# Performance work log

Hardware: AMD Instinct MI355X
Metric: run time of the kernel (lower is better)

Reference implementation:

```python
import jax, jax.numpy as jnp
import numpy as np

B, T, D, N, H = 2, 2048, 2048, 16, 128
WINDOW = 1024
SOFT_CAP = 50.0
K_MASK = -2.3819763e+38
MAX_WAVELENGTH = 10000


def apply_rope(x, positions, head_dim):
    # x: [B, T, N, H], positions: [B, T]
    fraction = 2.0 * jnp.arange(head_dim // 2, dtype=jnp.float32) / head_dim
    timescale = MAX_WAVELENGTH ** fraction                      # [H/2]
    sinusoid = positions[..., None].astype(jnp.float32) / timescale  # [B, T, H/2]
    sinusoid = sinusoid[..., None, :]                           # [B, T, 1, H/2]
    sin, cos = jnp.sin(sinusoid), jnp.cos(sinusoid)
    first, second = jnp.split(x, 2, axis=-1)
    out = jnp.concatenate([first * cos - second * sin,
                           second * cos + first * sin], axis=-1)
    return out.astype(x.dtype)


def setup_inputs() -> dict:
    key = jax.random.key(0)
    k1, k2, k3 = jax.random.split(key, 3)
    x = jax.random.normal(k1, (B, T, D), dtype=jnp.float32)
    w_qkv = jax.random.normal(k2, (3, N, D, H), dtype=jnp.float32) * (D ** -0.5)
    w_out = jax.random.normal(k3, (N, H, D), dtype=jnp.float32) * ((N * H) ** -0.5)
    segment_pos = jnp.broadcast_to(jnp.arange(T, dtype=jnp.int32), (B, T))
    # causal attention mask [B, T, S]
    causal = jnp.tril(jnp.ones((T, T), dtype=jnp.bool_))
    attn_mask = jnp.broadcast_to(causal, (B, T, T))
    return {"x": x, "w_qkv": w_qkv, "w_out": w_out,
            "segment_pos": segment_pos, "attn_mask": attn_mask}


def reference(x, w_qkv, w_out, segment_pos, attn_mask):
    # QKV projection: [3, B, T, N, H]
    q, k, v = jnp.einsum('BTD,SNDH->SBTNH', x, w_qkv)
    q = apply_rope(q, segment_pos, H) * (H ** -0.5)
    k = apply_rope(k, segment_pos, H)
    logits = jnp.einsum('BTNH,BSNH->BTNS', q, k)
    # soft cap
    logits = jnp.tanh(logits / SOFT_CAP) * SOFT_CAP
    # sliding-window mask combined with causal mask
    ones = jnp.ones_like(attn_mask)
    sliding = jnp.triu(ones, -WINDOW + 1) & jnp.tril(ones, WINDOW - 1)
    mask = sliding & attn_mask                                   # [B, T, S]
    padded = jnp.where(mask[:, :, None, :], logits, K_MASK)
    probs = jax.nn.softmax(padded, axis=-1).astype(k.dtype)
    encoded = jnp.einsum('BTNS,BSNH->BTNH', probs, v)
    return jnp.einsum('BTNH,NHD->BTD', encoded, w_out)
```

## Files before the change

### kernel.cpp

```cpp
#include <hip/hip_runtime.h>

#define B_ 2
#define T_ 2048
#define D_ 2048
#define N_ 16
#define H_ 128
constexpr int WIN = 1024;

typedef __attribute__((ext_vector_type(8))) short s16x8;
typedef __attribute__((ext_vector_type(4))) float f32x4;
typedef __attribute__((ext_vector_type(4))) unsigned short u16x4;

typedef const __attribute__((address_space(1))) void cglobal_void;
typedef __attribute__((address_space(3))) void lds_void;

__device__ __forceinline__ unsigned short f2b(float f) {
  union { float f; unsigned u; } v; v.f = f;
  unsigned r = v.u + 0x7FFFu + ((v.u >> 16) & 1u);
  return (unsigned short)(r >> 16);
}
__device__ __forceinline__ float b2f(unsigned short u) {
  union { unsigned u; float f; } v; v.u = ((unsigned)u) << 16;
  return v.f;
}

__global__ __launch_bounds__(256) void detect_kernel(
    const unsigned short* __restrict__ x, int* __restrict__ flag) {
  __shared__ int cnt[256];
  const int tid = threadIdx.x;
  int c = 0;
  for (int i = tid; i < 4096; i += 256) {
    const unsigned short u = x[2 * i];
    const int e = (u >> 7) & 0xFF;
    if (e >= 154) ++c;
  }
  cnt[tid] = c;
  __syncthreads();
  for (int s = 128; s > 0; s >>= 1) {
    if (tid < s) cnt[tid] += cnt[tid + s];
    __syncthreads();
  }
  if (tid == 0) *flag = cnt[0];
}

__global__ __launch_bounds__(256) void convert_x_kernel(
    const void* __restrict__ src, unsigned short* __restrict__ dst,
    const int* __restrict__ flag, int n4) {
  const int i = blockIdx.x * 256 + threadIdx.x;
  if (i >= n4) return;
  const bool isf = (*flag > 64);
  u16x4 o;
  if (isf) {
    const float4 f = ((const float4*)src)[i];
    o[0] = f2b(f.x); o[1] = f2b(f.y); o[2] = f2b(f.z); o[3] = f2b(f.w);
  } else {
    o = ((const u16x4*)src)[i];
  }
  *(u16x4*)(dst + 4 * (size_t)i) = o;
}

__global__ __launch_bounds__(256) void transpose_kernel(
    const void* __restrict__ src, unsigned short* __restrict__ dst,
    int R, int C, const int* __restrict__ flag) {
  __shared__ unsigned short tile[32][33];
  const bool isf = (*flag > 64);
  const int c0 = blockIdx.x * 32, r0 = blockIdx.y * 32;
  const size_t base = (size_t)blockIdx.z * R * C;
  const int tx = threadIdx.x, ty = threadIdx.y;
#pragma unroll
  for (int j = 0; j < 32; j += 8) {
    const size_t idx = base + (size_t)(r0 + ty + j) * C + c0 + tx;
    tile[ty + j][tx] = isf ? f2b(((const float*)src)[idx])
                           : ((const unsigned short*)src)[idx];
  }
  __syncthreads();
#pragma unroll
  for (int j = 0; j < 32; j += 8)
    dst[base + (size_t)(c0 + ty + j) * R + r0 + tx] = tile[tx][ty + j];
}

__global__ __launch_bounds__(256) void transpose_bf16_kernel(
    const unsigned short* __restrict__ src, unsigned short* __restrict__ dst,
    int R, int C) {
  __shared__ unsigned short tile[32][33];
  const int c0 = blockIdx.x * 32, r0 = blockIdx.y * 32;
  const size_t base = (size_t)blockIdx.z * R * C;
  const int tx = threadIdx.x, ty = threadIdx.y;
#pragma unroll
  for (int j = 0; j < 32; j += 8)
    tile[ty + j][tx] = src[base + (size_t)(r0 + ty + j) * C + c0 + tx];
  __syncthreads();
#pragma unroll
  for (int j = 0; j < 32; j += 8)
    dst[base + (size_t)(c0 + ty + j) * R + r0 + tx] = tile[tx][ty + j];
}

__global__ __launch_bounds__(512, 2) void gemm256_kernel(
    const unsigned short* __restrict__ A,
    const unsigned short* __restrict__ Bt,
    void* __restrict__ outp,
    int mode, const int* __restrict__ flag) {
  constexpr int K = D_;
  __shared__ unsigned short As[2][16384];
  __shared__ unsigned short Bs[2][16384];
  const int tid = threadIdx.x;
  const int lane = tid & 63;
  const int lr = lane & 15, lq = lane >> 4;
  const int wave = tid >> 6;
  const int wm = (wave >> 2) * 128, wn = (wave & 3) * 64;
  const size_t m0 = (size_t)blockIdx.x * 256;
  const unsigned short* pA = A + m0 * K;
  const unsigned short* pB = Bt + (size_t)blockIdx.y * 256 * K;

  const int fv = *flag;
  asm volatile("s_waitcnt vmcnt(0)" ::: "memory");

  const int cgs = (tid & 3) ^ ((tid >> 3) & 3);
  const size_t gbase = (size_t)(tid >> 2) * K + (size_t)(cgs * 8);

  const int swz = (lr >> 1) & 3;
  const int aoff = (wm + lr) * 32 + ((lq ^ swz) << 3);
  const int boff = (wn + lr) * 32 + ((lq ^ swz) << 3);

  f32x4 acc[8][4] = {};
  s16x8 af[8], bf[2];

#define STAGE(mat, ptr, ibuf, kk, h)                                          \
  {                                                                           \
    _Pragma("unroll")                                                         \
    for (int j = 0; j < 2; ++j)                                               \
      __builtin_amdgcn_global_load_lds(                                       \
          (cglobal_void*)((ptr) + gbase + (size_t)j * 128 * K + (kk) + (h) * 32), \
          (lds_void*)(&mat[ibuf][(h) * 8192 + (j * 512 + tid) * 8]), 16, 0, 0); \
  }

#define LOAD_A(kq)                                                            \
  {                                                                           \
    _Pragma("unroll")                                                         \
    for (int mb = 0; mb < 8; ++mb)                                            \
      af[mb] = *(const s16x8*)(&As[ib][(kq) * 8192 + aoff + mb * 512]);       \
  }

#define LOAD_B(kq, nh)                                                        \
  {                                                                           \
    _Pragma("unroll")                                                         \
    for (int nb = 0; nb < 2; ++nb)                                            \
      bf[nb] = *(const s16x8*)(&Bs[ib][(kq) * 8192 + boff + ((nh) * 2 + nb) * 512]); \
  }

#define PHASE_MID()                                                           \
  __builtin_amdgcn_s_barrier();                                               \
  asm volatile("s_waitcnt lgkmcnt(0)" ::: "memory");                          \
  __builtin_amdgcn_sched_barrier(0);

#define MFMA16(nh)                                                            \
  __builtin_amdgcn_s_setprio(1);                                              \
  {                                                                           \
    _Pragma("unroll")                                                         \
    for (int mb = 0; mb < 8; ++mb) {                                          \
      acc[mb][(nh) * 2] = __builtin_amdgcn_mfma_f32_16x16x32_bf16(            \
          af[mb], bf[0], acc[mb][(nh) * 2], 0, 0, 0);                         \
      acc[mb][(nh) * 2 + 1] = __builtin_amdgcn_mfma_f32_16x16x32_bf16(        \
          af[mb], bf[1], acc[mb][(nh) * 2 + 1], 0, 0, 0);                     \
    }                                                                         \
  }                                                                           \
  __builtin_amdgcn_s_setprio(0);

#define PHASE_END() __builtin_amdgcn_s_barrier();
#define VM4() asm volatile("s_waitcnt vmcnt(4)" ::: "memory");

  STAGE(As, pA, 0, 0, 0);
  STAGE(Bs, pB, 0, 0, 0);
  STAGE(As, pA, 0, 0, 1);
  STAGE(Bs, pB, 0, 0, 1);
  VM4();
  __builtin_amdgcn_s_barrier();

  for (int t = 0; t < K / 64; ++t) {
    const int ib = t & 1;
    const int kn = (t + 1) * 64;
    LOAD_A(0); LOAD_B(0, 0);
    STAGE(As, pA, ib ^ 1, kn, 0);
    PHASE_MID(); MFMA16(0); PHASE_END();
    LOAD_B(0, 1);
    STAGE(Bs, pB, ib ^ 1, kn, 0);
    VM4();
    PHASE_MID(); MFMA16(1); PHASE_END();
    LOAD_A(1); LOAD_B(1, 0);
    STAGE(As, pA, ib ^ 1, kn, 1);
    PHASE_MID(); MFMA16(0); PHASE_END();
    LOAD_B(1, 1);
    STAGE(Bs, pB, ib ^ 1, kn, 1);
    VM4();
    PHASE_MID(); MFMA16(1); PHASE_END();
  }

  const int n0 = blockIdx.y << 8;
  if (mode == 0) {
    const bool isf = (fv > 64);
#pragma unroll
    for (int mb = 0; mb < 8; ++mb) {
#pragma unroll
      for (int i = 0; i < 4; ++i) {
        const size_t r = m0 + wm + mb * 16 + lq * 4 + i;
#pragma unroll
        for (int nb = 0; nb < 4; ++nb) {
          const size_t c = (size_t)(n0 + wn + nb * 16 + lr);
          if (isf) ((float*)outp)[r * D_ + c] = acc[mb][nb][i];
          else ((unsigned short*)outp)[r * D_ + c] = f2b(acc[mb][nb][i]);
        }
      }
    }
  } else {
    unsigned short* op = (unsigned short*)outp;
    const size_t SB = (size_t)B_ * N_ * T_ * H_;
#pragma unroll
    for (int mb = 0; mb < 8; ++mb) {
#pragma unroll
      for (int i = 0; i < 4; ++i) {
        const size_t r = m0 + wm + mb * 16 + lq * 4 + i;
        const int b = (int)(r >> 11);
        const int tt = (int)(r & 2047);
#pragma unroll
        for (int nb = 0; nb < 4; ++nb) {
          const int g = n0 + wn + nb * 16 + lr;
          const int s = g >> 11, n = (g >> 7) & 15, h = g & 127;
          op[(size_t)s * SB + (size_t)(b * N_ + n) * T_ * H_ +
             (size_t)tt * H_ + h] = f2b(acc[mb][nb][i]);
        }
      }
    }
  }
#undef STAGE
#undef LOAD_A
#undef LOAD_B
#undef PHASE_MID
#undef MFMA16
#undef PHASE_END
#undef VM4
}

__global__ __launch_bounds__(512, 2) void gemm256x128_kernel(
    const unsigned short* __restrict__ A,
    const unsigned short* __restrict__ Bt,
    void* __restrict__ outp,
    int mode, const int* __restrict__ flag) {
  constexpr int K = D_;
  __shared__ unsigned short As[3 * 16384];
  __shared__ unsigned short Bs[3 * 8192];
  const int tid = threadIdx.x;
  const int lane = tid & 63;
  const int lr = lane & 15, lq = lane >> 4;
  const int wave = tid >> 6;
  const int wm = (wave >> 1) * 64, wn = (wave & 1) * 64;

  const int lin = blockIdx.y * 16 + blockIdx.x;
  const int nblk = (int)(gridDim.x * gridDim.y);
  const int wg = (lin & 7) * (nblk >> 3) + (lin >> 3);
  const int bx = wg & 15;
  const int by = wg >> 4;

  const size_t m0 = (size_t)bx * 256;
  const unsigned short* pA = A + m0 * K;
  const unsigned short* pB = Bt + (size_t)by * 128 * K;

  const int fv = *flag;
  asm volatile("s_waitcnt vmcnt(0)" ::: "memory");

  const int cgs = (tid & 3) ^ ((tid >> 3) & 3);
  const size_t gbase = (size_t)(tid >> 2) * K + (size_t)(cgs * 8);

  const int swz = (lr >> 1) & 3;
  const int aoff = (wm + lr) * 32 + ((lq ^ swz) << 3);
  const int boff = (wn + lr) * 32 + ((lq ^ swz) << 3);

  f32x4 acc[4][4] = {};
  s16x8 af[4], bf[4];

#define STAGE_A(bufp, kk, h)                                                  \
  {                                                                           \
    _Pragma("unroll")                                                         \
    for (int j = 0; j < 2; ++j)                                               \
      __builtin_amdgcn_global_load_lds(                                       \
          (cglobal_void*)(pA + gbase + (size_t)j * 128 * K + (kk) + (h) * 32),\
          (lds_void*)((bufp) + (h) * 8192 + (j * 512 + tid) * 8), 16, 0, 0);  \
  }
#define STAGE_B(bufp, kk, h)                                                  \
  __builtin_amdgcn_global_load_lds(                                           \
      (cglobal_void*)(pB + gbase + (kk) + (h) * 32),                          \
      (lds_void*)((bufp) + (h) * 4096 + tid * 8), 16, 0, 0);

#define LOAD_F(h)                                                             \
  {                                                                           \
    _Pragma("unroll")                                                         \
    for (int i = 0; i < 4; ++i) {                                             \
      af[i] = *(const s16x8*)(Ab + (h) * 8192 + aoff + i * 512);              \
      bf[i] = *(const s16x8*)(Bb + (h) * 4096 + boff + i * 512);              \
    }                                                                         \
  }

#define PHASE_MID()                                                           \
  __builtin_amdgcn_s_barrier();                                               \
  asm volatile("s_waitcnt lgkmcnt(0)" ::: "memory");                          \
  __builtin_amdgcn_sched_barrier(0);

#define MFMA16()                                                              \
  __builtin_amdgcn_s_setprio(1);                                              \
  {                                                                           \
    _Pragma("unroll")                                                         \
    for (int mb = 0; mb < 4; ++mb) {                                          \
      _Pragma("unroll")                                                       \
      for (int nb = 0; nb < 4; ++nb)                                          \
        acc[mb][nb] = __builtin_amdgcn_mfma_f32_16x16x32_bf16(                \
            af[mb], bf[nb], acc[mb][nb], 0, 0, 0);                            \
    }                                                                         \
  }                                                                           \
  __builtin_amdgcn_s_setprio(0);

#define PHASE_END() __builtin_amdgcn_s_barrier();
#define VM6() asm volatile("s_waitcnt vmcnt(6)" ::: "memory");

  STAGE_A(As, 0, 0); STAGE_A(As, 0, 1); STAGE_B(Bs, 0, 0); STAGE_B(Bs, 0, 1);
  STAGE_A(As + 16384, 64, 0); STAGE_A(As + 16384, 64, 1);
  STAGE_B(Bs + 8192, 64, 0);  STAGE_B(Bs + 8192, 64, 1);
  VM6();
  __builtin_amdgcn_s_barrier();

  int bt = 0, bp = 2;
  for (int t = 0; t < K / 64; ++t) {
    const unsigned short* Ab = As + bt * 16384;
    const unsigned short* Bb = Bs + bt * 8192;
    unsigned short* Ap = As + bp * 16384;
    unsigned short* Bp = Bs + bp * 8192;
    const int kn = (t + 2) * 64;
    LOAD_F(0);
    STAGE_A(Ap, kn, 0); STAGE_B(Bp, kn, 0);
    PHASE_MID(); MFMA16(); PHASE_END();
    LOAD_F(1);
    STAGE_A(Ap, kn, 1); STAGE_B(Bp, kn, 1);
    VM6();
    PHASE_MID(); MFMA16(); PHASE_END();
    bt = (bt == 2) ? 0 : bt + 1;
    bp = (bp == 2) ? 0 : bp + 1;
  }

  const int n0 = by << 7;
  if (mode == 0) {
    const bool isf = (fv > 64);
#pragma unroll
    for (int mb = 0; mb < 4; ++mb) {
#pragma unroll
      for (int i = 0; i < 4; ++i) {
        const size_t r = m0 + wm + mb * 16 + lq * 4 + i;
#pragma unroll
        for (int nb = 0; nb < 4; ++nb) {
          const size_t c = (size_t)(n0 + wn + nb * 16 + lr);
          if (isf) ((float*)outp)[r * D_ + c] = acc[mb][nb][i];
          else ((unsigned short*)outp)[r * D_ + c] = f2b(acc[mb][nb][i]);
        }
      }
    }
  } else {
    unsigned short* op = (unsigned short*)outp;
    const size_t SB = (size_t)B_ * N_ * T_ * H_;
#pragma unroll
    for (int mb = 0; mb < 4; ++mb) {
#pragma unroll
      for (int i = 0; i < 4; ++i) {
        const size_t r = m0 + wm + mb * 16 + lq * 4 + i;
        const int b = (int)(r >> 11);
        const int tt = (int)(r & 2047);
#pragma unroll
        for (int nb = 0; nb < 4; ++nb) {
          const int g = n0 + wn + nb * 16 + lr;
          const int s = g >> 11, n = (g >> 7) & 15, h = g & 127;
          op[(size_t)s * SB + (size_t)(b * N_ + n) * T_ * H_ +
             (size_t)tt * H_ + h] = f2b(acc[mb][nb][i]);
        }
      }
    }
  }
#undef STAGE_A
#undef STAGE_B
#undef LOAD_F
#undef PHASE_MID
#undef MFMA16
#undef PHASE_END
#undef VM6
}

__global__ __launch_bounds__(256) void rope_kernel(unsigned short* __restrict__ qk) {
  const int tid = threadIdx.x;
  const int lane = tid & 63;
  const size_t row = (size_t)blockIdx.x * 4 + (tid >> 6);
  const int t = (int)(row & (T_ - 1));
  const int s = (int)(row >> 16);
  unsigned short* p = qk + row * H_;
  float x1 = b2f(p[lane]), x2 = b2f(p[lane + 64]);
  const float inv_ts = exp2f(-0.20762050f * (float)lane);
  float sv, cv;
  __sincosf((float)t * inv_ts, &sv, &cv);
  float o1 = x1 * cv - x2 * sv;
  float o2 = x2 * cv + x1 * sv;
  if (s == 0) { o1 *= 0.08838834764831845f; o2 *= 0.08838834764831845f; }
  p[lane] = f2b(o1);
  p[lane + 64] = f2b(o2);
}

__global__ __launch_bounds__(256, 2) void attn_kernel(
    const unsigned short* __restrict__ qkv,
    const unsigned short* __restrict__ vt,
    unsigned short* __restrict__ enc) {
  const int tid = threadIdx.x, lane = tid & 63, wave = tid >> 6;
  const int lr = lane & 15, lq = lane >> 4;
  const int bn = blockIdx.x;
  const int b = bn >> 4, n = bn & 15;
  const int t0 = blockIdx.y * 64;
  const size_t SB = (size_t)B_ * N_ * T_ * H_;
  const unsigned short* qp = qkv + (size_t)bn * T_ * H_;
  const unsigned short* kp = qp + SB;
  const unsigned short* vp = vt + (size_t)bn * T_ * H_;

  __shared__ unsigned short Ks[2][64 * 128];
  __shared__ unsigned short Vt[2][128 * 64];
  __shared__ unsigned short Psm[4][16 * 64];
  unsigned short* Ps = Psm[wave];

  const int cgK = (tid & 15) ^ ((tid >> 4) & 15);
  const int cgV = (tid & 7) ^ ((tid >> 3) & 7);
  size_t goffK[4], goffV[4];
#pragma unroll
  for (int j = 0; j < 4; ++j) {
    goffK[j] = (size_t)(j * 16 + (tid >> 4)) * H_ + cgK * 8;
    goffV[j] = (size_t)(j * 32 + (tid >> 3)) * T_ + cgV * 8;
  }

  s16x8 aq[4];
  {
    const int t = t0 + wave * 16 + lr;
#pragma unroll
    for (int kc = 0; kc < 4; ++kc)
      aq[kc] = *(const s16x8*)(qp + (size_t)t * H_ + kc * 32 + lq * 8);
  }
  asm volatile("s_waitcnt vmcnt(0)" ::: "memory");

#define STAGE_T(ibuf, s0v)                                                    \
  {                                                                           \
    _Pragma("unroll")                                                         \
    for (int j = 0; j < 4; ++j) {                                             \
      __builtin_amdgcn_global_load_lds(                                       \
          (cglobal_void*)(kp + (size_t)(s0v) * H_ + goffK[j]),                \
          (lds_void*)(Ks[ibuf] + (size_t)(j * 256 + tid) * 8), 16, 0, 0);     \
      __builtin_amdgcn_global_load_lds(                                       \
          (cglobal_void*)(vp + goffV[j] + (s0v)),                             \
          (lds_void*)(Vt[ibuf] + (size_t)(j * 256 + tid) * 8), 16, 0, 0);     \
    }                                                                         \
  }

  f32x4 oacc[8] = {};
  float lp[4] = {0.f, 0.f, 0.f, 0.f};

  const int s_lo = (t0 >= WIN - 1) ? ((t0 - (WIN - 1)) & ~63) : 0;
  constexpr float C_IN = 0.05770780f;
  constexpr float M_SCALE = -144.269504f;
  constexpr float M_BIAS = 86.56f;

  STAGE_T(0, s_lo);

  int cur = 0;
  for (int s0 = s_lo; s0 <= t0 + 63; s0 += 64) {
    STAGE_T(cur ^ 1, s0 + 64);
    asm volatile("s_waitcnt vmcnt(8)" ::: "memory");
    __builtin_amdgcn_s_barrier();

    const unsigned short* Kb = Ks[cur];
    const unsigned short* Vb = Vt[cur];

    float p[4][4];
#pragma unroll
    for (int sb = 0; sb < 4; ++sb) {
      f32x4 a = {};
#pragma unroll
      for (int kc = 0; kc < 4; ++kc) {
        const int co = (((kc << 2) + lq) ^ lr) * 8;
        s16x8 bk = *(const s16x8*)(Kb + (sb * 16 + lr) * 128 + co);
        a = __builtin_amdgcn_mfma_f32_16x16x32_bf16(aq[kc], bk, a, 0, 0, 0);
      }
#pragma unroll
      for (int i = 0; i < 4; ++i) {
        const float u = exp2f(a[i] * C_IN);
        const float r = __builtin_amdgcn_rcpf(u + 1.0f);
        p[sb][i] = exp2f(fmaf(r, M_SCALE, M_BIAS));
      }
    }

    const bool interior = (s0 + 63 <= t0) && (s0 >= t0 + 63 - (WIN - 1));
    if (!interior) {
#pragma unroll
      for (int sb = 0; sb < 4; ++sb) {
        const int key = s0 + sb * 16 + lr;
#pragma unroll
        for (int i = 0; i < 4; ++i) {
          const int t = t0 + wave * 16 + lq * 4 + i;
          if (key > t || key < t - (WIN - 1)) p[sb][i] = 0.0f;
        }
      }
    }
#pragma unroll
    for (int sb = 0; sb < 4; ++sb)
#pragma unroll
      for (int i = 0; i < 4; ++i) lp[i] += p[sb][i];

#pragma unroll
    for (int sb = 0; sb < 4; ++sb)
#pragma unroll
      for (int i = 0; i < 4; ++i) {
        const int row = lq * 4 + i;
        const int cph = ((sb * 2 + (lr >> 3)) ^ (row & 7));
        Ps[row * 64 + cph * 8 + (lr & 7)] = f2b(p[sb][i]);
      }

    s16x8 ap[2];
#pragma unroll
    for (int kc = 0; kc < 2; ++kc)
      ap[kc] = *(const s16x8*)(Ps + lr * 64 + ((((kc << 2) + lq) ^ (lr & 7)) * 8));

#pragma unroll
    for (int hb = 0; hb < 8; ++hb) {
#pragma unroll
      for (int kc = 0; kc < 2; ++kc) {
        const int co = (((kc << 2) + lq) ^ (lr & 7)) * 8;
        s16x8 bv = *(const s16x8*)(Vb + (hb * 16 + lr) * 64 + co);
        oacc[hb] = __builtin_amdgcn_mfma_f32_16x16x32_bf16(ap[kc], bv, oacc[hb], 0, 0, 0);
      }
    }

    __builtin_amdgcn_s_barrier();
    cur ^= 1;
  }
#undef STAGE_T

#pragma unroll
  for (int i = 0; i < 4; ++i) {
#pragma unroll
    for (int off = 1; off < 16; off <<= 1)
      lp[i] += __shfl_xor(lp[i], off, 64);
  }

#pragma unroll
  for (int i = 0; i < 4; ++i) {
    const int t = t0 + wave * 16 + lq * 4 + i;
    const float inv = 1.0f / lp[i];
    const size_t rowb = ((size_t)b * T_ + t) * (N_ * H_) + (size_t)n * H_;
#pragma unroll
    for (int hb = 0; hb < 8; ++hb)
      enc[rowb + hb * 16 + lr] = f2b(oacc[hb][i] * inv);
  }
}

extern "C" void kernel_launch(void* const* d_in, const int* in_sizes, int n_in,
                              void* d_out, int out_size, void* d_ws, size_t ws_size,
                              hipStream_t stream) {
  const void* x     = d_in[0];
  const void* w_qkv = d_in[1];
  const void* w_out = d_in[2];

  char* wsb = (char*)d_ws;
  int* flag = (int*)wsb;
  const size_t MB = 1048576;
  unsigned short* xc    = (unsigned short*)(wsb + 64);
  unsigned short* wqkvT = (unsigned short*)(wsb + 64 + 16 * MB);
  unsigned short* qkv   = (unsigned short*)(wsb + 64 + 40 * MB);
  unsigned short* vt    = xc;
  unsigned short* enc   = wqkvT;
  unsigned short* woutT = (unsigned short*)(wsb + 64 + 32 * MB);
  unsigned short* v     = qkv + 2 * (size_t)B_ * N_ * T_ * H_;

  detect_kernel<<<1, 256, 0, stream>>>((const unsigned short*)x, flag);
  convert_x_kernel<<<8192, 256, 0, stream>>>(x, xc, flag, B_ * T_ * D_ / 4);
  transpose_kernel<<<dim3(4, 64, 48), dim3(32, 8), 0, stream>>>(w_qkv, wqkvT, 2048, 128, flag);
  gemm256_kernel<<<dim3(16, 24), 512, 0, stream>>>(xc, wqkvT, qkv, 1, flag);
  rope_kernel<<<32768, 256, 0, stream>>>(qkv);
  transpose_bf16_kernel<<<dim3(4, 64, 32), dim3(32, 8), 0, stream>>>(v, vt, 2048, 128);
  transpose_kernel<<<dim3(64, 64, 1), dim3(32, 8), 0, stream>>>(w_out, woutT, 2048, 2048, flag);
  attn_kernel<<<dim3(32, 32), 256, 0, stream>>>(qkv, vt, enc);
  gemm256x128_kernel<<<dim3(16, 16), 512, 0, stream>>>(enc, woutT, d_out, 0, flag);
}
```

Measured before the change: 431.5 us.

## Rebalance GEMM fragment loads and drop explicit LDS waitcnt/sched barriers

The 256x256 GEMM now splits each k-quarter into two 4x4 MFMA halves over the M dimension. Each half uses 4 A fragments and 4 B fragments, where before it used all 8 A fragments with 2 B fragments per N-half. This evens out the LDS reads per phase and lowers fragment register pressure. Both GEMM kernels also drop the explicit lgkmcnt(0) wait and sched_barrier in the middle of each phase and leave LDS-read waits to the compiler, so loads can overlap MFMAs more freely. The risk is that the compiler inserts waits or reorders work less favourably than the hand-placed barriers did.

```diff
diff --git a/kernel.cpp b/kernel.cpp
--- a/kernel.cpp
+++ b/kernel.cpp
@@ -123,7 +123,7 @@
   const int boff = (wn + lr) * 32 + ((lq ^ swz) << 3);
 
   f32x4 acc[8][4] = {};
-  s16x8 af[8], bf[2];
+  s16x8 af[4], bf[4];
 
 #define STAGE(mat, ptr, ibuf, kk, h)                                          \
   {                                                                           \
@@ -134,39 +134,34 @@
           (lds_void*)(&mat[ibuf][(h) * 8192 + (j * 512 + tid) * 8]), 16, 0, 0); \
   }
 
-#define LOAD_A(kq)                                                            \
-  {                                                                           \
-    _Pragma("unroll")                                                         \
-    for (int mb = 0; mb < 8; ++mb)                                            \
-      af[mb] = *(const s16x8*)(&As[ib][(kq) * 8192 + aoff + mb * 512]);       \
-  }
-
-#define LOAD_B(kq, nh)                                                        \
-  {                                                                           \
-    _Pragma("unroll")                                                         \
-    for (int nb = 0; nb < 2; ++nb)                                            \
-      bf[nb] = *(const s16x8*)(&Bs[ib][(kq) * 8192 + boff + ((nh) * 2 + nb) * 512]); \
-  }
-
-#define PHASE_MID()                                                           \
-  __builtin_amdgcn_s_barrier();                                               \
-  asm volatile("s_waitcnt lgkmcnt(0)" ::: "memory");                          \
-  __builtin_amdgcn_sched_barrier(0);
-
-#define MFMA16(nh)                                                            \
+#define LOAD_AF(kq, mh)                                                       \
+  {                                                                           \
+    _Pragma("unroll")                                                         \
+    for (int i = 0; i < 4; ++i)                                               \
+      af[i] = *(const s16x8*)(&As[ib][(kq) * 8192 + aoff + ((mh) * 4 + i) * 512]); \
+  }
+
+#define LOAD_BF(kq)                                                           \
+  {                                                                           \
+    _Pragma("unroll")                                                         \
+    for (int nb = 0; nb < 4; ++nb)                                            \
+      bf[nb] = *(const s16x8*)(&Bs[ib][(kq) * 8192 + boff + nb * 512]);       \
+  }
+
+#define MFMA16(mh)                                                            \
   __builtin_amdgcn_s_setprio(1);                                              \
   {                                                                           \
     _Pragma("unroll")                                                         \
-    for (int mb = 0; mb < 8; ++mb) {                                          \
-      acc[mb][(nh) * 2] = __builtin_amdgcn_mfma_f32_16x16x32_bf16(            \
-          af[mb], bf[0], acc[mb][(nh) * 2], 0, 0, 0);                         \
-      acc[mb][(nh) * 2 + 1] = __builtin_amdgcn_mfma_f32_16x16x32_bf16(        \
-          af[mb], bf[1], acc[mb][(nh) * 2 + 1], 0, 0, 0);                     \
+    for (int mb = 0; mb < 4; ++mb) {                                          \
+      _Pragma("unroll")                                                       \
+      for (int nb = 0; nb < 4; ++nb)                                          \
+        acc[(mh) * 4 + mb][nb] = __builtin_amdgcn_mfma_f32_16x16x32_bf16(     \
+            af[mb], bf[nb], acc[(mh) * 4 + mb][nb], 0, 0, 0);                 \
     }                                                                         \
   }                                                                           \
   __builtin_amdgcn_s_setprio(0);
 
-#define PHASE_END() __builtin_amdgcn_s_barrier();
+#define BAR() __builtin_amdgcn_s_barrier();
 #define VM4() asm volatile("s_waitcnt vmcnt(4)" ::: "memory");
 
   STAGE(As, pA, 0, 0, 0);
@@ -174,25 +169,25 @@
   STAGE(As, pA, 0, 0, 1);
   STAGE(Bs, pB, 0, 0, 1);
   VM4();
-  __builtin_amdgcn_s_barrier();
+  BAR();
 
   for (int t = 0; t < K / 64; ++t) {
     const int ib = t & 1;
     const int kn = (t + 1) * 64;
-    LOAD_A(0); LOAD_B(0, 0);
+    LOAD_AF(0, 0); LOAD_BF(0);
     STAGE(As, pA, ib ^ 1, kn, 0);
-    PHASE_MID(); MFMA16(0); PHASE_END();
-    LOAD_B(0, 1);
+    BAR(); MFMA16(0); BAR();
+    LOAD_AF(0, 1);
     STAGE(Bs, pB, ib ^ 1, kn, 0);
     VM4();
-    PHASE_MID(); MFMA16(1); PHASE_END();
-    LOAD_A(1); LOAD_B(1, 0);
+    BAR(); MFMA16(1); BAR();
+    LOAD_AF(1, 0); LOAD_BF(1);
     STAGE(As, pA, ib ^ 1, kn, 1);
-    PHASE_MID(); MFMA16(0); PHASE_END();
-    LOAD_B(1, 1);
+    BAR(); MFMA16(0); BAR();
+    LOAD_AF(1, 1);
     STAGE(Bs, pB, ib ^ 1, kn, 1);
     VM4();
-    PHASE_MID(); MFMA16(1); PHASE_END();
+    BAR(); MFMA16(1); BAR();
   }
 
   const int n0 = blockIdx.y << 8;
@@ -232,11 +227,10 @@
     }
   }
 #undef STAGE
-#undef LOAD_A
-#undef LOAD_B
-#undef PHASE_MID
+#undef LOAD_AF
+#undef LOAD_BF
 #undef MFMA16
-#undef PHASE_END
+#undef BAR
 #undef VM4
 }
 
@@ -299,11 +293,6 @@
     }                                                                         \
   }
 
-#define PHASE_MID()                                                           \
-  __builtin_amdgcn_s_barrier();                                               \
-  asm volatile("s_waitcnt lgkmcnt(0)" ::: "memory");                          \
-  __builtin_amdgcn_sched_barrier(0);
-
 #define MFMA16()                                                              \
   __builtin_amdgcn_s_setprio(1);                                              \
   {                                                                           \
@@ -317,14 +306,14 @@
   }                                                                           \
   __builtin_amdgcn_s_setprio(0);
 
-#define PHASE_END() __builtin_amdgcn_s_barrier();
+#define BAR() __builtin_amdgcn_s_barrier();
 #define VM6() asm volatile("s_waitcnt vmcnt(6)" ::: "memory");
 
   STAGE_A(As, 0, 0); STAGE_A(As, 0, 1); STAGE_B(Bs, 0, 0); STAGE_B(Bs, 0, 1);
   STAGE_A(As + 16384, 64, 0); STAGE_A(As + 16384, 64, 1);
   STAGE_B(Bs + 8192, 64, 0);  STAGE_B(Bs + 8192, 64, 1);
   VM6();
-  __builtin_amdgcn_s_barrier();
+  BAR();
 
   int bt = 0, bp = 2;
   for (int t = 0; t < K / 64; ++t) {
@@ -335,11 +324,11 @@
     const int kn = (t + 2) * 64;
     LOAD_F(0);
     STAGE_A(Ap, kn, 0); STAGE_B(Bp, kn, 0);
-    PHASE_MID(); MFMA16(); PHASE_END();
+    BAR(); MFMA16(); BAR();
     LOAD_F(1);
     STAGE_A(Ap, kn, 1); STAGE_B(Bp, kn, 1);
     VM6();
-    PHASE_MID(); MFMA16(); PHASE_END();
+    BAR(); MFMA16(); BAR();
     bt = (bt == 2) ? 0 : bt + 1;
     bp = (bp == 2) ? 0 : bp + 1;
   }
@@ -383,9 +372,8 @@
 #undef STAGE_A
 #undef STAGE_B
 #undef LOAD_F
-#undef PHASE_MID
 #undef MFMA16
-#undef PHASE_END
+#undef BAR
 #undef VM6
 }
 
```

Result: no change. 435.7 us (+1.0%).
